# Kernel tuning notes

Measured on AMD Instinct MI355X. Metric: run time of the kernel, lower is better.

Reference implementation:

```python
import jax, jax.numpy as jnp
import numpy as np

IN_DIM = 128
DIM = 32

def setup_inputs() -> dict:
    key = jax.random.key(0)
    ks = jax.random.split(key, 7)
    b, r, L = 1, 128, 256
    m = jax.random.normal(ks[0], (b, r, L, IN_DIM), dtype=jnp.float32)
    ln_w = jnp.ones((IN_DIM,), dtype=jnp.float32)
    ln_b = jnp.zeros((IN_DIM,), dtype=jnp.float32)
    W1 = jax.random.normal(ks[1], (2 * DIM, IN_DIM), dtype=jnp.float32) / np.sqrt(IN_DIM)
    b1 = jax.random.normal(ks[2], (2 * DIM,), dtype=jnp.float32) * 0.01
    W2 = jax.random.normal(ks[3], (IN_DIM, DIM * DIM), dtype=jnp.float32) / np.sqrt(DIM * DIM)
    b2 = jax.random.normal(ks[4], (IN_DIM,), dtype=jnp.float32) * 0.01
    return {"m": m, "ln_w": ln_w, "ln_b": ln_b, "W1": W1, "b1": b1, "W2": W2, "b2": b2}

def reference(m, ln_w, ln_b, W1, b1, W2, b2):
    nrow = m.shape[1]
    # LayerNorm over last dim
    mu = jnp.mean(m, axis=-1, keepdims=True)
    var = jnp.var(m, axis=-1, keepdims=True)
    mn = (m - mu) / jnp.sqrt(var + 1e-5) * ln_w + ln_b
    # projection to a, b (chunk on last dim)
    proj = jnp.einsum('bric,fc->brif', mn, W1) + b1  # [b,r,L,2*DIM]
    a, bb = proj[..., :DIM], proj[..., DIM:]
    # outer-product mean over rows r
    out = jnp.einsum('bric,brjd->bijcd', a, bb) / nrow  # [b,L,L,DIM,DIM]
    B, I, J = out.shape[0], out.shape[1], out.shape[2]
    out = out.reshape(B, I, J, DIM * DIM)
    z = jnp.einsum('bijk,fk->bijf', out, W2) + b2  # [b,L,L,IN_DIM]
    return z
```

## Files before the change

kernel.cpp:

```cpp
#include <hip/hip_runtime.h>
#include <stdint.h>

typedef __attribute__((ext_vector_type(8))) short  short8;
typedef __attribute__((ext_vector_type(4))) float  f32x4;

static __device__ __forceinline__ uint16_t f2bf(float x) {
    union { float f; uint32_t u; } v; v.f = x;
    return (uint16_t)((v.u + 0x7FFFu + ((v.u >> 16) & 1u)) >> 16);
}


__global__ __launch_bounds__(256) void prep_weights(
    const float* __restrict__ W2, const float* __restrict__ W1,
    uint16_t* __restrict__ W2f, uint16_t* __restrict__ W1f) {
    int bid = blockIdx.x, t = threadIdx.x;
    if (bid < 512) {
        int idx = bid * 256 + t;
        int f  = idx >> 10;
        int kd = idx & 1023;
        int d = kd >> 5, c = kd & 31;
        int ftile = f >> 4, l16 = f & 15;
        int ks = kd >> 5, kh = (kd >> 3) & 3, e = kd & 7;
        W2f[(size_t)(ftile * 32 + ks) * 512 + (l16 + 16 * kh) * 8 + e] =
            f2bf(W2[f * 1024 + c * 32 + d]);
    } else {
        int idx = (bid - 512) * 256 + t;
        int f = idx >> 7, c = idx & 127;
        int ftile = f >> 4, l16 = f & 15;
        int ks = c >> 5, kh = (c >> 3) & 3, e = c & 7;
        W1f[(size_t)(ftile * 4 + ks) * 512 + (l16 + 16 * kh) * 8 + e] =
            f2bf(W1[f * 128 + c]);
    }
}

__global__ __launch_bounds__(256) void ln_proj(
    const float* __restrict__ mI, const float* __restrict__ lnw,
    const float* __restrict__ lnb, const uint16_t* __restrict__ W1f,
    const float* __restrict__ b1,
    uint16_t* __restrict__ At, uint16_t* __restrict__ Bt)
{
    __shared__ __align__(16) uint16_t mns[256 * 8];
    const int t = threadIdx.x;
    const int bid = blockIdx.x;
    const int i0 = (bid * 16) & 255;
    const int r  = bid >> 4;

    {
        int row = t >> 4, cb = t & 15;
        const float* rp = mI + ((size_t)bid * 16 + row) * 128 + cb * 8;
        float4 v0 = *(const float4*)(rp);
        float4 v1 = *(const float4*)(rp + 4);
        float s  = v0.x + v0.y + v0.z + v0.w + v1.x + v1.y + v1.z + v1.w;
        float ss = v0.x*v0.x + v0.y*v0.y + v0.z*v0.z + v0.w*v0.w
                 + v1.x*v1.x + v1.y*v1.y + v1.z*v1.z + v1.w*v1.w;
        #pragma unroll
        for (int off = 8; off > 0; off >>= 1) {
            s  += __shfl_xor(s, off);
            ss += __shfl_xor(ss, off);
        }
        float mean = s * (1.0f / 128.0f);
        float var  = ss * (1.0f / 128.0f) - mean * mean;
        float rstd = rsqrtf(var + 1e-5f);
        float4 wa = *(const float4*)(lnw + cb * 8);
        float4 wb = *(const float4*)(lnw + cb * 8 + 4);
        float4 ba = *(const float4*)(lnb + cb * 8);
        float4 bb = *(const float4*)(lnb + cb * 8 + 4);
        uint16_t y[8];
        y[0] = f2bf((v0.x - mean) * rstd * wa.x + ba.x);
        y[1] = f2bf((v0.y - mean) * rstd * wa.y + ba.y);
        y[2] = f2bf((v0.z - mean) * rstd * wa.z + ba.z);
        y[3] = f2bf((v0.w - mean) * rstd * wa.w + ba.w);
        y[4] = f2bf((v1.x - mean) * rstd * wb.x + bb.x);
        y[5] = f2bf((v1.y - mean) * rstd * wb.y + bb.y);
        y[6] = f2bf((v1.z - mean) * rstd * wb.z + bb.z);
        y[7] = f2bf((v1.w - mean) * rstd * wb.w + bb.w);
        int g = cb * 16 + (row ^ (cb & 7));
        *(uint2*)&mns[g * 8]     = *(uint2*)&y[0];
        *(uint2*)&mns[g * 8 + 4] = *(uint2*)&y[4];
    }
    __syncthreads();

    const int w = t >> 6, l = t & 63;
    const int l16 = l & 15, lh = l >> 4;
    f32x4 acc = (f32x4)(0.0f);
    #pragma unroll
    for (int ks = 0; ks < 4; ++ks) {
        int cb = ks * 4 + lh;
        int g  = cb * 16 + (l16 ^ (cb & 7));
        short8 a = *(const short8*)&mns[g * 8];
        short8 b = *(const short8*)(W1f + (size_t)(w * 4 + ks) * 512 + l * 8);
        acc = __builtin_amdgcn_mfma_f32_16x16x32_bf16(a, b, acc, 0, 0, 0);
    }
    float b1v = b1[w * 16 + l16];
    uint16_t* dst = (w < 2) ? At : Bt;
    const float scale = (w < 2) ? (1.0f / 128.0f) : 1.0f;
    const int cch = w & 1;
    const int base2 = (r >> 5) * 512 + (l16 + 16 * ((r >> 3) & 3)) * 8 + (r & 7);
    #pragma unroll
    for (int v = 0; v < 4; ++v) {
        int i = i0 + lh * 4 + v;
        int mtile = i * 2 + cch;
        dst[(size_t)mtile * 2048 + base2] = f2bf((acc[v] + b1v) * scale);
    }
}

extern __shared__ uint16_t outl[];
__global__ __launch_bounds__(512, 4) void fused_opm(
    const uint16_t* __restrict__ At, const uint16_t* __restrict__ Bt,
    const uint16_t* __restrict__ W2f, const float* __restrict__ b2,
    float* __restrict__ z)
{
    const int t = threadIdx.x;
    const int w = t >> 6, l = t & 63;
    const int l16 = l & 15, lh = l >> 4;
    const int bx = blockIdx.x, by = blockIdx.y;
    const int wm = w >> 1, wn = w & 1;

    f32x4 acc[4][4];
    #pragma unroll
    for (int a = 0; a < 4; ++a)
        #pragma unroll
        for (int b = 0; b < 4; ++b) acc[a][b] = (f32x4)(0.0f);

    const uint16_t* Abase = At + (size_t)(by * 16 + wm * 4) * 4 * 512 + l * 8;
    const uint16_t* Bbase = Bt + (size_t)(bx * 8 + wn * 4) * 4 * 512 + l * 8;
    #pragma unroll
    for (int ks = 0; ks < 4; ++ks) {
        short8 af[4], bf[4];
        #pragma unroll
        for (int mt = 0; mt < 4; ++mt)
            af[mt] = *(const short8*)(Abase + (size_t)(mt * 4 + ks) * 512);
        #pragma unroll
        for (int nt = 0; nt < 4; ++nt)
            bf[nt] = *(const short8*)(Bbase + (size_t)(nt * 4 + ks) * 512);
        #pragma unroll
        for (int mt = 0; mt < 4; ++mt)
            #pragma unroll
            for (int nt = 0; nt < 4; ++nt)
                acc[mt][nt] = __builtin_amdgcn_mfma_f32_16x16x32_bf16(
                    af[mt], bf[nt], acc[mt][nt], 0, 0, 0);
    }

    const uint16_t* Wt = W2f + (size_t)w * 32 * 512 + l * 8;
    short8 wb[4];
    #pragma unroll
    for (int q = 0; q < 4; ++q)
        wb[q] = *(const short8*)(Wt + (size_t)q * 512);

    #pragma unroll
    for (int mt = 0; mt < 4; ++mt) {
        const int kh = (mt & 1) * 2 + (lh >> 1);
        const int e0 = (lh & 1) * 4;
        #pragma unroll
        for (int nt = 0; nt < 4; ++nt) {
            int p  = wm * 8 + (mt >> 1) * 4 + wn * 2 + (nt >> 1);
            int ks = (nt & 1) * 16 + l16;
            int pt = p >> 4, l16t = p & 15;
            f32x4 v = acc[mt][nt];
            uint32_t u0 = (uint32_t)f2bf(v[0]) | ((uint32_t)f2bf(v[1]) << 16);
            uint32_t u1 = (uint32_t)f2bf(v[2]) | ((uint32_t)f2bf(v[3]) << 16);
            uint32_t byte = (uint32_t)(pt * 32 + ks) * 1024u
                          + (uint32_t)(l16t + 16 * kh) * 16u + (uint32_t)e0 * 2u;
            byte ^= (uint32_t)(ks & 7) << 4;
            uint2 pk; pk.x = u0; pk.y = u1;
            *(uint2*)((char*)outl + byte) = pk;
        }
    }
    __syncthreads();

    f32x4 zacc[2][2];
    #pragma unroll
    for (int a = 0; a < 2; ++a) { zacc[a][0] = (f32x4)(0.0f); zacc[a][1] = (f32x4)(0.0f); }

    #pragma unroll
    for (int ks = 0; ks < 32; ++ks) {
        short8 cw = wb[ks & 3];
        if (ks < 28) wb[ks & 3] = *(const short8*)(Wt + (size_t)(ks + 4) * 512);
        uint32_t swz = (uint32_t)(ks & 7) << 4;
        uint32_t o0b = ((uint32_t)ks * 1024u + (uint32_t)l * 16u) ^ swz;
        uint32_t o1b = ((uint32_t)(32 + ks) * 1024u + (uint32_t)l * 16u) ^ swz;
        short8 o0 = *(const short8*)((const char*)outl + o0b);
        short8 o1 = *(const short8*)((const char*)outl + o1b);
        zacc[0][ks & 1] = __builtin_amdgcn_mfma_f32_16x16x32_bf16(cw, o0, zacc[0][ks & 1], 0, 0, 0);
        zacc[1][ks & 1] = __builtin_amdgcn_mfma_f32_16x16x32_bf16(cw, o1, zacc[1][ks & 1], 0, 0, 0);
    }

    const int f0 = w * 16 + lh * 4;
    const float4 bv = *(const float4*)(b2 + f0);
    #pragma unroll
    for (int pt = 0; pt < 2; ++pt) {
        int p  = pt * 16 + l16;
        int zi = by * 8 + (p >> 2);
        int zj = bx * 4 + (p & 3);
        float* zrow = z + ((size_t)zi * 256 + zj) * 128;
        float4 zr;
        zr.x = zacc[pt][0][0] + zacc[pt][1][0] + bv.x;
        zr.y = zacc[pt][0][1] + zacc[pt][1][1] + bv.y;
        zr.z = zacc[pt][0][2] + zacc[pt][1][2] + bv.z;
        zr.w = zacc[pt][0][3] + zacc[pt][1][3] + bv.w;
        *(float4*)(zrow + f0) = zr;
    }
}

extern "C" void kernel_launch(void* const* d_in, const int* in_sizes, int n_in,
                              void* d_out, int out_size, void* d_ws, size_t ws_size,
                              hipStream_t stream) {
    const float* m_in = (const float*)d_in[0];
    const float* ln_w = (const float*)d_in[1];
    const float* ln_b = (const float*)d_in[2];
    const float* W1   = (const float*)d_in[3];
    const float* b1   = (const float*)d_in[4];
    const float* W2   = (const float*)d_in[5];
    const float* b2   = (const float*)d_in[6];
    float* z = (float*)d_out;

    uint16_t* At  = (uint16_t*)d_ws;
    uint16_t* Bt  = At + 8192 * 128;
    uint16_t* W2f = Bt + 8192 * 128;
    uint16_t* W1f = W2f + 128 * 1024;

    prep_weights<<<544, 256, 0, stream>>>(W2, W1, W2f, W1f);
    ln_proj<<<2048, 256, 0, stream>>>(m_in, ln_w, ln_b, W1f, b1, At, Bt);
    fused_opm<<<dim3(64, 32), 512, 64 * 1024, stream>>>(At, Bt, W2f, b2, z);
}
```

Measured before the change: 64.16 us.

## Use 32x32x16 MFMA for W2 projection with split-K across warp halves

Rewrites the second GEMM stage (outer product times W2) to use 32x32x16 bf16 MFMA instead of 16x16x32. W2 is repacked for the new operand layout, and the outer-product tile is stored in LDS with a new swizzle. Each half of the warps computes half of the K dimension, and the partial sums are reduced through LDS. This adds an extra barrier and LDS round trip in exchange for fewer, larger MFMA instructions and fewer LDS reads per output.

```diff
diff --git a/kernel.cpp b/kernel.cpp
--- a/kernel.cpp
+++ b/kernel.cpp
@@ -1,12 +1,13 @@
 #include <hip/hip_runtime.h>
 #include <stdint.h>
 
-typedef __attribute__((ext_vector_type(8))) short  short8;
-typedef __attribute__((ext_vector_type(4))) float  f32x4;
-
-static __device__ __forceinline__ uint16_t f2bf(float x) {
+typedef __attribute__((ext_vector_type(8)))  short short8;
+typedef __attribute__((ext_vector_type(4)))  float f32x4;
+typedef __attribute__((ext_vector_type(16))) float f32x16;
+
+static __device__ __forceinline__ uint32_t f2bf(float x) {
     union { float f; uint32_t u; } v; v.f = x;
-    return (uint16_t)((v.u + 0x7FFFu + ((v.u >> 16) & 1u)) >> 16);
+    return (v.u + 0x7FFFu + ((v.u >> 16) & 1u)) >> 16;
 }
 
 
@@ -19,17 +20,17 @@
         int f  = idx >> 10;
         int kd = idx & 1023;
         int d = kd >> 5, c = kd & 31;
-        int ftile = f >> 4, l16 = f & 15;
-        int ks = kd >> 5, kh = (kd >> 3) & 3, e = kd & 7;
-        W2f[(size_t)(ftile * 32 + ks) * 512 + (l16 + 16 * kh) * 8 + e] =
-            f2bf(W2[f * 1024 + c * 32 + d]);
+        int ft = f >> 5, r32 = f & 31;
+        int ks16 = kd >> 4, kh32 = (kd >> 3) & 1, e = kd & 7;
+        W2f[(size_t)(ft * 64 + ks16) * 512 + (r32 + 32 * kh32) * 8 + e] =
+            (uint16_t)f2bf(W2[f * 1024 + c * 32 + d]);
     } else {
         int idx = (bid - 512) * 256 + t;
         int f = idx >> 7, c = idx & 127;
         int ftile = f >> 4, l16 = f & 15;
         int ks = c >> 5, kh = (c >> 3) & 3, e = c & 7;
         W1f[(size_t)(ftile * 4 + ks) * 512 + (l16 + 16 * kh) * 8 + e] =
-            f2bf(W1[f * 128 + c]);
+            (uint16_t)f2bf(W1[f * 128 + c]);
     }
 }
 
@@ -66,14 +67,14 @@
         float4 ba = *(const float4*)(lnb + cb * 8);
         float4 bb = *(const float4*)(lnb + cb * 8 + 4);
         uint16_t y[8];
-        y[0] = f2bf((v0.x - mean) * rstd * wa.x + ba.x);
-        y[1] = f2bf((v0.y - mean) * rstd * wa.y + ba.y);
-        y[2] = f2bf((v0.z - mean) * rstd * wa.z + ba.z);
-        y[3] = f2bf((v0.w - mean) * rstd * wa.w + ba.w);
-        y[4] = f2bf((v1.x - mean) * rstd * wb.x + bb.x);
-        y[5] = f2bf((v1.y - mean) * rstd * wb.y + bb.y);
-        y[6] = f2bf((v1.z - mean) * rstd * wb.z + bb.z);
-        y[7] = f2bf((v1.w - mean) * rstd * wb.w + bb.w);
+        y[0] = (uint16_t)f2bf((v0.x - mean) * rstd * wa.x + ba.x);
+        y[1] = (uint16_t)f2bf((v0.y - mean) * rstd * wa.y + ba.y);
+        y[2] = (uint16_t)f2bf((v0.z - mean) * rstd * wa.z + ba.z);
+        y[3] = (uint16_t)f2bf((v0.w - mean) * rstd * wa.w + ba.w);
+        y[4] = (uint16_t)f2bf((v1.x - mean) * rstd * wb.x + bb.x);
+        y[5] = (uint16_t)f2bf((v1.y - mean) * rstd * wb.y + bb.y);
+        y[6] = (uint16_t)f2bf((v1.z - mean) * rstd * wb.z + bb.z);
+        y[7] = (uint16_t)f2bf((v1.w - mean) * rstd * wb.w + bb.w);
         int g = cb * 16 + (row ^ (cb & 7));
         *(uint2*)&mns[g * 8]     = *(uint2*)&y[0];
         *(uint2*)&mns[g * 8 + 4] = *(uint2*)&y[4];
@@ -100,7 +101,7 @@
     for (int v = 0; v < 4; ++v) {
         int i = i0 + lh * 4 + v;
         int mtile = i * 2 + cch;
-        dst[(size_t)mtile * 2048 + base2] = f2bf((acc[v] + b1v) * scale);
+        dst[(size_t)mtile * 2048 + base2] = (uint16_t)f2bf((acc[v] + b1v) * scale);
     }
 }
 
@@ -141,64 +142,80 @@
                     af[mt], bf[nt], acc[mt][nt], 0, 0, 0);
     }
 
-    const uint16_t* Wt = W2f + (size_t)w * 32 * 512 + l * 8;
-    short8 wb[4];
+    const int h32 = w >> 2;
+    const int ft  = w & 3;
+    const uint16_t* Wt = W2f + ((size_t)ft * 64 + (size_t)h32 * 32) * 512 + l * 8;
+    short8 wbuf[4];
     #pragma unroll
     for (int q = 0; q < 4; ++q)
-        wb[q] = *(const short8*)(Wt + (size_t)q * 512);
-
-    #pragma unroll
-    for (int mt = 0; mt < 4; ++mt) {
-        const int kh = (mt & 1) * 2 + (lh >> 1);
-        const int e0 = (lh & 1) * 4;
-        #pragma unroll
-        for (int nt = 0; nt < 4; ++nt) {
-            int p  = wm * 8 + (mt >> 1) * 4 + wn * 2 + (nt >> 1);
-            int ks = (nt & 1) * 16 + l16;
-            int pt = p >> 4, l16t = p & 15;
-            f32x4 v = acc[mt][nt];
-            uint32_t u0 = (uint32_t)f2bf(v[0]) | ((uint32_t)f2bf(v[1]) << 16);
-            uint32_t u1 = (uint32_t)f2bf(v[2]) | ((uint32_t)f2bf(v[3]) << 16);
-            uint32_t byte = (uint32_t)(pt * 32 + ks) * 1024u
-                          + (uint32_t)(l16t + 16 * kh) * 16u + (uint32_t)e0 * 2u;
-            byte ^= (uint32_t)(ks & 7) << 4;
-            uint2 pk; pk.x = u0; pk.y = u1;
-            *(uint2*)((char*)outl + byte) = pk;
+        wbuf[q] = *(const short8*)(Wt + (size_t)q * 512);
+
+    {
+        const int kh32w = lh >> 1;
+        const uint32_t e0b = (uint32_t)((lh & 1) * 4) * 2u;
+        #pragma unroll
+        for (int mt = 0; mt < 4; ++mt) {
+            #pragma unroll
+            for (int nt = 0; nt < 4; ++nt) {
+                int p    = wm * 8 + (mt >> 1) * 4 + wn * 2 + (nt >> 1);
+                int d    = (nt & 1) * 16 + l16;
+                int ks16 = 2 * d + (mt & 1);
+                f32x4 v = acc[mt][nt];
+                uint2 pk;
+                pk.x = f2bf(v[0]) | (f2bf(v[1]) << 16);
+                pk.y = f2bf(v[2]) | (f2bf(v[3]) << 16);
+                uint32_t off = (uint32_t)(p + 32 * kh32w) * 16u + e0b;
+                off ^= ((uint32_t)((ks16 & 7) ^ kh32w)) << 4;
+                *(uint2*)((char*)outl + (uint32_t)ks16 * 1024u + off) = pk;
+            }
         }
     }
     __syncthreads();
 
-    f32x4 zacc[2][2];
-    #pragma unroll
-    for (int a = 0; a < 2; ++a) { zacc[a][0] = (f32x4)(0.0f); zacc[a][1] = (f32x4)(0.0f); }
-
-    #pragma unroll
-    for (int ks = 0; ks < 32; ++ks) {
-        short8 cw = wb[ks & 3];
-        if (ks < 28) wb[ks & 3] = *(const short8*)(Wt + (size_t)(ks + 4) * 512);
-        uint32_t swz = (uint32_t)(ks & 7) << 4;
-        uint32_t o0b = ((uint32_t)ks * 1024u + (uint32_t)l * 16u) ^ swz;
-        uint32_t o1b = ((uint32_t)(32 + ks) * 1024u + (uint32_t)l * 16u) ^ swz;
-        short8 o0 = *(const short8*)((const char*)outl + o0b);
-        short8 o1 = *(const short8*)((const char*)outl + o1b);
-        zacc[0][ks & 1] = __builtin_amdgcn_mfma_f32_16x16x32_bf16(cw, o0, zacc[0][ks & 1], 0, 0, 0);
-        zacc[1][ks & 1] = __builtin_amdgcn_mfma_f32_16x16x32_bf16(cw, o1, zacc[1][ks & 1], 0, 0, 0);
-    }
-
-    const int f0 = w * 16 + lh * 4;
-    const float4 bv = *(const float4*)(b2 + f0);
-    #pragma unroll
-    for (int pt = 0; pt < 2; ++pt) {
-        int p  = pt * 16 + l16;
-        int zi = by * 8 + (p >> 2);
-        int zj = bx * 4 + (p & 3);
+    f32x16 zacc0 = (f32x16)(0.0f), zacc1 = (f32x16)(0.0f);
+    const int kh32r = l >> 5;
+    #pragma unroll
+    for (int it = 0; it < 32; ++it) {
+        short8 cw = wbuf[it & 3];
+        if (it < 28) wbuf[it & 3] = *(const short8*)(Wt + (size_t)(it + 4) * 512);
+        int ks16 = h32 * 32 + it;
+        uint32_t off = ((uint32_t)l * 16u) ^ (((uint32_t)((ks16 & 7) ^ kh32r)) << 4);
+        short8 o = *(const short8*)((const char*)outl + (uint32_t)ks16 * 1024u + off);
+        if (it & 1) zacc1 = __builtin_amdgcn_mfma_f32_32x32x16_bf16(cw, o, zacc1, 0, 0, 0);
+        else        zacc0 = __builtin_amdgcn_mfma_f32_32x32x16_bf16(cw, o, zacc0, 0, 0, 0);
+    }
+
+    float part[16];
+    #pragma unroll
+    for (int rr = 0; rr < 16; ++rr) part[rr] = zacc0[rr] + zacc1[rr];
+
+    __syncthreads();
+    float* red = (float*)outl;
+    if (w >= 4) {
+        #pragma unroll
+        for (int rr = 0; rr < 16; ++rr)
+            red[(ft * 16 + rr) * 64 + l] = part[rr];
+    }
+    __syncthreads();
+    if (w < 4) {
+        #pragma unroll
+        for (int rr = 0; rr < 16; ++rr)
+            part[rr] += red[(ft * 16 + rr) * 64 + l];
+        const int p  = l & 31;
+        const int zi = by * 8 + (p >> 2);
+        const int zj = bx * 4 + (p & 3);
         float* zrow = z + ((size_t)zi * 256 + zj) * 128;
-        float4 zr;
-        zr.x = zacc[pt][0][0] + zacc[pt][1][0] + bv.x;
-        zr.y = zacc[pt][0][1] + zacc[pt][1][1] + bv.y;
-        zr.z = zacc[pt][0][2] + zacc[pt][1][2] + bv.z;
-        zr.w = zacc[pt][0][3] + zacc[pt][1][3] + bv.w;
-        *(float4*)(zrow + f0) = zr;
+        #pragma unroll
+        for (int rq = 0; rq < 4; ++rq) {
+            int f0 = ft * 32 + rq * 8 + 4 * (l >> 5);
+            float4 bv = *(const float4*)(b2 + f0);
+            float4 zr;
+            zr.x = part[rq * 4 + 0] + bv.x;
+            zr.y = part[rq * 4 + 1] + bv.y;
+            zr.z = part[rq * 4 + 2] + bv.z;
+            zr.w = part[rq * 4 + 3] + bv.w;
+            *(float4*)(zrow + f0) = zr;
+        }
     }
 }
 
```

New measurement: 69.75 us. 1.09x slower.
